# Kernel tuning notes

Measured on AMD Instinct MI355X. Metric: run time of the kernel, lower is better.

Reference implementation:

```python
import jax, jax.numpy as jnp
import numpy as np

HIDDEN = 128
EDGE_DIM = 32
N_NODES = 50000
N_EDGES = 800000


def setup_inputs() -> dict:
    key = jax.random.key(0)
    ks = jax.random.split(key, 8)
    node_features = jax.random.normal(ks[0], (N_NODES, HIDDEN), dtype=jnp.float32)
    edge_index = jax.random.randint(ks[1], (2, N_EDGES), 0, N_NODES, dtype=jnp.int64)
    edge_attr = jax.random.normal(ks[2], (N_EDGES, EDGE_DIM), dtype=jnp.float32)
    # parameters (Linear stored as [in, out] for x @ W + b)
    s_et = 1.0 / np.sqrt(EDGE_DIM)
    W_edge = jax.random.uniform(ks[3], (EDGE_DIM, HIDDEN), jnp.float32, -s_et, s_et)
    b_edge = jnp.zeros((HIDDEN,), jnp.float32)
    s1 = 1.0 / np.sqrt(3 * HIDDEN)
    W1 = jax.random.uniform(ks[4], (3 * HIDDEN, HIDDEN), jnp.float32, -s1, s1)
    b1 = jnp.zeros((HIDDEN,), jnp.float32)
    s2 = 1.0 / np.sqrt(HIDDEN)
    W2 = jax.random.uniform(ks[5], (HIDDEN, 1), jnp.float32, -s2, s2)
    b2 = jnp.zeros((1,), jnp.float32)
    return {
        "node_features": node_features,
        "edge_attr": edge_attr,
        "W_edge": W_edge, "b_edge": b_edge,
        "W1": W1, "b1": b1, "W2": W2, "b2": b2,
        "edge_index": edge_index,
    }


def reference(node_features, edge_attr, W_edge, b_edge, W1, b1, W2, b2, edge_index):
    row, col = edge_index[0], edge_index[1]
    src = node_features[row]                 # [E, H] gather
    dst = node_features[col]                 # [E, H] gather
    edge_feat = edge_attr @ W_edge + b_edge  # [E, H]
    combined = jnp.concatenate([src, edge_feat, dst], axis=-1)  # [E, 3H]
    h = jax.nn.relu(combined @ W1 + b1)      # [E, H]
    attn = jax.nn.sigmoid(h @ W2 + b2)       # [E, 1]
    return attn
```

## Files before the change

kernel.cpp:

```cpp
#include <hip/hip_runtime.h>
#include <hip/hip_bf16.h>

#define HIDDEN   128
#define EDGE_DIM 32
#define NNODE    50000
#define NEDGE    800000
#define KSTEPS   9
#define NFRAG    8
#define LDS_KS   8

typedef __attribute__((ext_vector_type(4))) float        f32x4;
typedef __attribute__((ext_vector_type(8))) short        bf16x8;
typedef __attribute__((ext_vector_type(4))) unsigned int u32x4;

#define BPACK_USHORTS  (KSTEPS * NFRAG * 64 * 8)
#define BIAS_OFF_BYTES (BPACK_USHORTS * 2)
#define FLAG_OFF_BYTES (BIAS_OFF_BYTES + 128 * 4)
#define DATA_OFF       74752

#define PP_OFF   DATA_OFF
#define QP_OFF   (PP_OFF + NNODE * HIDDEN * 2)
#define IDXN_OFF (QP_OFF + NNODE * HIDDEN * 2)
#define WS_NEW   (IDXN_OFF + 2 * NEDGE * 4)

#define NODE_OFF_BYTES DATA_OFF
#define IDX_OFF_BYTES  (NODE_OFF_BYTES + NNODE * HIDDEN * 2)
#define WS_R8          (IDX_OFF_BYTES + 2 * NEDGE * 4)

__device__ __forceinline__ unsigned short f2bf(float f) {
  unsigned u = __builtin_bit_cast(unsigned, f);
  u += 0x7FFFu + ((u >> 16) & 1u);
  return (unsigned short)(u >> 16);
}

__device__ __forceinline__ unsigned cvt_pk_bf16(float a, float b) {
  union { __hip_bfloat162 h; unsigned u; } cv;
  cv.h = __float22bfloat162_rn(make_float2(a, b));
  return cv.u;
}

__device__ __forceinline__ bf16x8 pack8(f32x4 lo, f32x4 hi) {
  u32x4 u;
  u[0] = cvt_pk_bf16(lo[0], lo[1]);
  u[1] = cvt_pk_bf16(lo[2], lo[3]);
  u[2] = cvt_pk_bf16(hi[0], hi[1]);
  u[3] = cvt_pk_bf16(hi[2], hi[3]);
  return __builtin_bit_cast(bf16x8, u);
}

__device__ __forceinline__ void gload_lds16(const void* g, void* l) {
  __builtin_amdgcn_global_load_lds(
      (const __attribute__((address_space(1))) unsigned int*)g,
      (__attribute__((address_space(3))) unsigned int*)l, 16, 0, 0);
}

#define MFMA(a, b, c) __builtin_amdgcn_mfma_f32_16x16x32_bf16((a), (b), (c), 0, 0, 0)

__global__ void setup_kernel(const float* __restrict__ W_edge,
                             const float* __restrict__ b_edge,
                             const float* __restrict__ W1,
                             const float* __restrict__ b1,
                             const void*  __restrict__ eidx,
                             unsigned short* __restrict__ Bpack,
                             float* __restrict__ bias_eff,
                             int*   __restrict__ flag64) {
  const int bid = blockIdx.x, tid = threadIdx.x;
  if (bid < 36) {
    const int pair  = bid * 2 + (tid >> 6);
    const int lane  = tid & 63;
    const int kstep = pair >> 3;
    const int f     = pair & 7;
    const int col   = f * 16 + (lane & 15);
    const int kbase = kstep * 32 + (lane >> 4) * 8;
    float vals[8];
#pragma unroll
    for (int j = 0; j < 8; ++j) {
      const int k = kbase + j;
      float val;
      if (k < 128) {
        val = W1[k * 128 + col];
      } else if (k < 256) {
        val = W1[(k + 128) * 128 + col];
      } else {
        const int kk = k - 256;
        float s = 0.f;
        for (int t = 0; t < 128; ++t)
          s = fmaf(W_edge[kk * 128 + t], W1[(128 + t) * 128 + col], s);
        val = s;
      }
      vals[j] = val;
    }
    u32x4 sv;
#pragma unroll
    for (int j = 0; j < 4; ++j)
      sv[j] = (unsigned)f2bf(vals[2 * j]) | ((unsigned)f2bf(vals[2 * j + 1]) << 16);
    *(u32x4*)(Bpack + ((kstep * NFRAG + f) * 64 + lane) * 8) = sv;
  } else {
    if (tid < 128) {
      float s = b1[tid];
      for (int t = 0; t < 128; ++t)
        s = fmaf(b_edge[t], W1[(128 + t) * 128 + tid], s);
      bias_eff[tid] = s;
    }
    if (tid == 0) {
      const unsigned* w = (const unsigned*)eidx;
      int all0 = 1;
      for (int i = 0; i < 64; ++i) all0 &= (w[2 * i + 1] == 0u) ? 1 : 0;
      *flag64 = all0;
    }
  }
}

__global__ __launch_bounds__(256) void cvt_nodes_kernel(const float* __restrict__ nodef,
                                                        unsigned short* __restrict__ nbf) {
  const int i = blockIdx.x * 256 + threadIdx.x;
  if (i >= NNODE * HIDDEN / 8) return;
  f32x4 lo = *(const f32x4*)(nodef + i * 8);
  f32x4 hi = *(const f32x4*)(nodef + i * 8 + 4);
  *(bf16x8*)(nbf + i * 8) = pack8(lo, hi);
}

__global__ __launch_bounds__(256) void cvt_idx_kernel(const void* __restrict__ eidx,
                                                      const int* __restrict__ flag64,
                                                      int* __restrict__ idx32) {
  const int i = blockIdx.x * 256 + threadIdx.x;
  if (i >= 2 * NEDGE) return;
  if (*flag64) idx32[i] = (int)((const long long*)eidx)[i];
  else         idx32[i] = ((const int*)eidx)[i];
}

__global__ __launch_bounds__(256, 3) void pq_kernel(
    const float* __restrict__ nodef,
    const unsigned short* __restrict__ Bpack,
    const float* __restrict__ bias_eff,
    unsigned* __restrict__ Pp,
    unsigned* __restrict__ Qp) {
  const int tid  = threadIdx.x;
  const int lane = tid & 63;
  const int wid  = tid >> 6;
  const int l15  = lane & 15;
  const int kg   = lane >> 4;
  const int nb   = blockIdx.x * 128 + wid * 32;

  const int n0 = min(nb + l15, NNODE - 1);
  const int n1 = min(nb + 16 + l15, NNODE - 1);
  bf16x8 a0[4], a1[4];
#pragma unroll
  for (int ks = 0; ks < 4; ++ks) {
    const float* p0 = nodef + (size_t)n0 * HIDDEN + ks * 32 + kg * 8;
    const float* p1 = nodef + (size_t)n1 * HIDDEN + ks * 32 + kg * 8;
    a0[ks] = pack8(*(const f32x4*)p0, *(const f32x4*)(p0 + 4));
    a1[ks] = pack8(*(const f32x4*)p1, *(const f32x4*)(p1 + 4));
  }

  float bv[NFRAG];
#pragma unroll
  for (int f = 0; f < NFRAG; ++f) bv[f] = bias_eff[f * 16 + l15];

  f32x4 acc[2][NFRAG];
#pragma unroll
  for (int m = 0; m < 2; ++m)
#pragma unroll
    for (int f = 0; f < NFRAG; ++f)
      acc[m][f] = (f32x4){bv[f], bv[f], bv[f], bv[f]};
#pragma unroll
  for (int ks = 0; ks < 4; ++ks)
#pragma unroll
    for (int f = 0; f < NFRAG; ++f) {
      bf16x8 bfr = *(const bf16x8*)(Bpack + ((ks * NFRAG + f) * 64 + lane) * 8);
      acc[0][f] = MFMA(a0[ks], bfr, acc[0][f]);
      acc[1][f] = MFMA(a1[ks], bfr, acc[1][f]);
    }
#pragma unroll
  for (int m = 0; m < 2; ++m)
#pragma unroll
    for (int r = 0; r < 4; ++r) {
      const int n = nb + m * 16 + kg * 4 + r;
      if (n < NNODE) {
        u32x4 sv;
#pragma unroll
        for (int k = 0; k < 4; ++k)
          sv[k] = cvt_pk_bf16(acc[m][2 * k][r], acc[m][2 * k + 1][r]);
        *(u32x4*)(Pp + (size_t)n * 64 + l15 * 4) = sv;
      }
    }

#pragma unroll
  for (int m = 0; m < 2; ++m)
#pragma unroll
    for (int f = 0; f < NFRAG; ++f)
      acc[m][f] = (f32x4){0.f, 0.f, 0.f, 0.f};
#pragma unroll
  for (int ks = 0; ks < 4; ++ks)
#pragma unroll
    for (int f = 0; f < NFRAG; ++f) {
      bf16x8 bfr = *(const bf16x8*)(Bpack + (((ks + 4) * NFRAG + f) * 64 + lane) * 8);
      acc[0][f] = MFMA(a0[ks], bfr, acc[0][f]);
      acc[1][f] = MFMA(a1[ks], bfr, acc[1][f]);
    }
#pragma unroll
  for (int m = 0; m < 2; ++m)
#pragma unroll
    for (int r = 0; r < 4; ++r) {
      const int n = nb + m * 16 + kg * 4 + r;
      if (n < NNODE) {
        u32x4 sv;
#pragma unroll
        for (int k = 0; k < 4; ++k)
          sv[k] = cvt_pk_bf16(acc[m][2 * k][r], acc[m][2 * k + 1][r]);
        *(u32x4*)(Qp + (size_t)n * 64 + l15 * 4) = sv;
      }
    }
}

__global__ __launch_bounds__(256, 3) void edge_attn_pq(
    const float* __restrict__ eattr,
    const int*   __restrict__ idx32,
    const unsigned* __restrict__ Pp,
    const unsigned* __restrict__ Qp,
    const unsigned short* __restrict__ Bpack,
    const float* __restrict__ W2,
    const float* __restrict__ b2,
    float* __restrict__ out) {
  const int tid   = threadIdx.x;
  const int lane  = tid & 63;
  const int wid   = tid >> 6;
  const int l15   = lane & 15;
  const int kg    = lane >> 4;
  const int ebase = blockIdx.x * 128 + wid * 32;

  const f32x4 zero4 = {0.f, 0.f, 0.f, 0.f};

  int rn[2][4], cn[2][4];
#pragma unroll
  for (int m = 0; m < 2; ++m)
#pragma unroll
    for (int r = 0; r < 4; ++r) {
      rn[m][r] = idx32[ebase + m * 16 + kg * 4 + r];
      cn[m][r] = idx32[NEDGE + ebase + m * 16 + kg * 4 + r];
    }

  u32x4 pu[2][4], qu[2][4];
#pragma unroll
  for (int m = 0; m < 2; ++m)
#pragma unroll
    for (int r = 0; r < 4; ++r)
      pu[m][r] = *(const u32x4*)(Pp + (size_t)rn[m][r] * 64 + l15 * 4);
#pragma unroll
  for (int m = 0; m < 2; ++m)
#pragma unroll
    for (int r = 0; r < 4; ++r)
      qu[m][r] = *(const u32x4*)(Qp + (size_t)cn[m][r] * 64 + l15 * 4);

  bf16x8 ae0, ae1;
  {
    const float* pe = eattr + (size_t)(ebase + l15) * EDGE_DIM + kg * 8;
    ae0 = pack8(*(const f32x4*)pe, *(const f32x4*)(pe + 4));
  }
  {
    const float* pe = eattr + (size_t)(ebase + 16 + l15) * EDGE_DIM + kg * 8;
    ae1 = pack8(*(const f32x4*)pe, *(const f32x4*)(pe + 4));
  }

  float w2v[NFRAG];
#pragma unroll
  for (int f = 0; f < NFRAG; ++f) w2v[f] = W2[f * 16 + l15];
  const float bias2 = b2[0];

  f32x4 acc[2][NFRAG];
#pragma unroll
  for (int f = 0; f < NFRAG; ++f) {
    bf16x8 bfr = *(const bf16x8*)(Bpack + ((8 * NFRAG + f) * 64 + lane) * 8);
    acc[0][f] = MFMA(ae0, bfr, zero4);
    acc[1][f] = MFMA(ae1, bfr, zero4);
  }

#pragma unroll
  for (int m = 0; m < 2; ++m)
#pragma unroll
    for (int r = 0; r < 4; ++r)
#pragma unroll
      for (int k = 0; k < 4; ++k) {
        const unsigned up = pu[m][r][k];
        acc[m][2 * k][r]     += __builtin_bit_cast(float, up << 16);
        acc[m][2 * k + 1][r] += __builtin_bit_cast(float, up & 0xffff0000u);
      }
#pragma unroll
  for (int m = 0; m < 2; ++m)
#pragma unroll
    for (int r = 0; r < 4; ++r)
#pragma unroll
      for (int k = 0; k < 4; ++k) {
        const unsigned uq = qu[m][r][k];
        acc[m][2 * k][r]     += __builtin_bit_cast(float, uq << 16);
        acc[m][2 * k + 1][r] += __builtin_bit_cast(float, uq & 0xffff0000u);
      }

  float part[2][4];
#pragma unroll
  for (int m = 0; m < 2; ++m)
#pragma unroll
    for (int rr = 0; rr < 4; ++rr) {
      float s = 0.f;
#pragma unroll
      for (int f = 0; f < NFRAG; ++f) {
        float h = fmaxf(acc[m][f][rr], 0.f);
        s = fmaf(h, w2v[f], s);
      }
      part[m][rr] = s;
    }

#pragma unroll
  for (int mask = 1; mask < 16; mask <<= 1)
#pragma unroll
    for (int m = 0; m < 2; ++m)
#pragma unroll
      for (int rr = 0; rr < 4; ++rr)
        part[m][rr] += __shfl_xor(part[m][rr], mask, 64);

  if (l15 == 0) {
#pragma unroll
    for (int m = 0; m < 2; ++m)
#pragma unroll
      for (int rr = 0; rr < 4; ++rr) {
        float x = part[m][rr] + bias2;
        out[ebase + m * 16 + kg * 4 + rr] = 1.f / (1.f + __expf(-x));
      }
  }
}

__global__ __launch_bounds__(512, 4) void edge_attn_kernel(
    const unsigned short* __restrict__ nbf,
    const float* __restrict__ eattr,
    const int*   __restrict__ idx32,
    const unsigned short* __restrict__ Bpack,
    const float* __restrict__ bias_eff,
    const float* __restrict__ W2,
    const float* __restrict__ b2,
    float* __restrict__ out) {
  __shared__ unsigned short lds_b[LDS_KS * NFRAG * 64 * 8];

  const int tid   = threadIdx.x;
  const int lane  = tid & 63;
  const int wid   = tid >> 6;
  const int l15   = lane & 15;
  const int kg    = lane >> 4;
  const int ebase = blockIdx.x * 256 + wid * 32;

#pragma unroll
  for (int i = 0; i < 8; ++i) {
    const char* g = (const char*)Bpack + (size_t)(i * 512 + tid) * 16;
    char*       l = (char*)lds_b + (size_t)(i * 512 + wid * 64) * 16;
    gload_lds16(g, l);
  }

  const int r0 = idx32[ebase + l15];
  const int r1 = idx32[ebase + 16 + l15];
  const int c0 = idx32[NEDGE + ebase + l15];
  const int c1 = idx32[NEDGE + ebase + 16 + l15];

  bf16x8 a0[4], a1[4];
#pragma unroll
  for (int ks = 0; ks < 4; ++ks) {
    a0[ks] = *(const bf16x8*)(nbf + (size_t)r0 * HIDDEN + kg * 8 + ks * 32);
    a1[ks] = *(const bf16x8*)(nbf + (size_t)r1 * HIDDEN + kg * 8 + ks * 32);
  }

  __syncthreads();

  f32x4 acc[2][NFRAG];
#pragma unroll
  for (int m = 0; m < 2; ++m)
#pragma unroll
    for (int f = 0; f < NFRAG; ++f)
      acc[m][f] = (f32x4){0.f, 0.f, 0.f, 0.f};

#pragma unroll
  for (int ks = 0; ks < 4; ++ks)
#pragma unroll
    for (int f = 0; f < NFRAG; ++f) {
      bf16x8 bfr = *(const bf16x8*)(lds_b + ((ks * NFRAG + f) * 64 + lane) * 8);
      acc[0][f] = MFMA(a0[ks], bfr, acc[0][f]);
      acc[1][f] = MFMA(a1[ks], bfr, acc[1][f]);
    }

  __builtin_amdgcn_sched_barrier(0);

#pragma unroll
  for (int ks = 0; ks < 4; ++ks) {
    a0[ks] = *(const bf16x8*)(nbf + (size_t)c0 * HIDDEN + kg * 8 + ks * 32);
    a1[ks] = *(const bf16x8*)(nbf + (size_t)c1 * HIDDEN + kg * 8 + ks * 32);
  }

#pragma unroll
  for (int ks = 0; ks < 4; ++ks)
#pragma unroll
    for (int f = 0; f < NFRAG; ++f) {
      bf16x8 bfr = *(const bf16x8*)(lds_b + (((ks + 4) * NFRAG + f) * 64 + lane) * 8);
      acc[0][f] = MFMA(a0[ks], bfr, acc[0][f]);
      acc[1][f] = MFMA(a1[ks], bfr, acc[1][f]);
    }

  __builtin_amdgcn_sched_barrier(0);

  bf16x8 ae0, ae1;
  {
    const float* pe = eattr + (size_t)(ebase + l15) * EDGE_DIM + kg * 8;
    ae0 = pack8(*(const f32x4*)pe, *(const f32x4*)(pe + 4));
  }
  {
    const float* pe = eattr + (size_t)(ebase + 16 + l15) * EDGE_DIM + kg * 8;
    ae1 = pack8(*(const f32x4*)pe, *(const f32x4*)(pe + 4));
  }
#pragma unroll
  for (int f = 0; f < NFRAG; ++f) {
    bf16x8 bfr = *(const bf16x8*)(Bpack + ((8 * NFRAG + f) * 64 + lane) * 8);
    acc[0][f] = MFMA(ae0, bfr, acc[0][f]);
    acc[1][f] = MFMA(ae1, bfr, acc[1][f]);
  }

  float w2v[NFRAG], bv[NFRAG];
#pragma unroll
  for (int f = 0; f < NFRAG; ++f) {
    w2v[f] = W2[f * 16 + l15];
    bv[f]  = bias_eff[f * 16 + l15];
  }
  const float bias2 = b2[0];

  float part[2][4];
#pragma unroll
  for (int m = 0; m < 2; ++m)
#pragma unroll
    for (int rr = 0; rr < 4; ++rr) {
      float s = 0.f;
#pragma unroll
      for (int f = 0; f < NFRAG; ++f) {
        float h = fmaxf(acc[m][f][rr] + bv[f], 0.f);
        s = fmaf(h, w2v[f], s);
      }
      part[m][rr] = s;
    }

#pragma unroll
  for (int mask = 1; mask < 16; mask <<= 1)
#pragma unroll
    for (int m = 0; m < 2; ++m)
#pragma unroll
      for (int rr = 0; rr < 4; ++rr)
        part[m][rr] += __shfl_xor(part[m][rr], mask, 64);

  if (l15 == 0) {
#pragma unroll
    for (int m = 0; m < 2; ++m)
#pragma unroll
      for (int rr = 0; rr < 4; ++rr) {
        float x = part[m][rr] + bias2;
        out[ebase + m * 16 + kg * 4 + rr] = 1.f / (1.f + __expf(-x));
      }
  }
}

__global__ __launch_bounds__(256) void edge_attn_kernel_fp32(
    const float* __restrict__ nodef,
    const float* __restrict__ eattr,
    const void*  __restrict__ eidx,
    const unsigned short* __restrict__ Bpack,
    const float* __restrict__ bias_eff,
    const float* __restrict__ W2,
    const float* __restrict__ b2,
    const int*   __restrict__ flag64,
    float* __restrict__ out) {
  const int lane  = threadIdx.x & 63;
  const int wid   = threadIdx.x >> 6;
  const int ebase = blockIdx.x * 128 + wid * 32;
  const int l15   = lane & 15;
  const int kg    = lane >> 4;
  const int koff  = kg * 8;
  const int e0 = ebase + l15;
  const int e1 = e0 + 16;

  long r0, c0, r1, c1;
  if (*flag64) {
    const long long* p = (const long long*)eidx;
    r0 = (long)p[e0];          r1 = (long)p[e1];
    c0 = (long)p[NEDGE + e0];  c1 = (long)p[NEDGE + e1];
  } else {
    const int* p = (const int*)eidx;
    r0 = p[e0];          r1 = p[e1];
    c0 = p[NEDGE + e0];  c1 = p[NEDGE + e1];
  }

  f32x4 acc[2][NFRAG];
#pragma unroll
  for (int m = 0; m < 2; ++m)
#pragma unroll
    for (int f = 0; f < NFRAG; ++f)
      acc[m][f] = (f32x4){0.f, 0.f, 0.f, 0.f};

#pragma unroll 1
  for (int ks = 0; ks < KSTEPS; ++ks) {
    const float *p0, *p1;
    if (ks < 4)      { p0 = nodef + r0 * HIDDEN + ks * 32;       p1 = nodef + r1 * HIDDEN + ks * 32; }
    else if (ks < 8) { p0 = nodef + c0 * HIDDEN + (ks - 4) * 32; p1 = nodef + c1 * HIDDEN + (ks - 4) * 32; }
    else             { p0 = eattr + (long)e0 * EDGE_DIM;         p1 = eattr + (long)e1 * EDGE_DIM; }

    f32x4 lo0 = *(const f32x4*)(p0 + koff);
    f32x4 hi0 = *(const f32x4*)(p0 + koff + 4);
    f32x4 lo1 = *(const f32x4*)(p1 + koff);
    f32x4 hi1 = *(const f32x4*)(p1 + koff + 4);
    bf16x8 a0 = pack8(lo0, hi0);
    bf16x8 a1 = pack8(lo1, hi1);

#pragma unroll
    for (int f = 0; f < NFRAG; ++f) {
      bf16x8 bfr = *(const bf16x8*)(Bpack + ((ks * NFRAG + f) * 64 + lane) * 8);
      acc[0][f] = MFMA(a0, bfr, acc[0][f]);
      acc[1][f] = MFMA(a1, bfr, acc[1][f]);
    }
  }

  float w2v[NFRAG], bv[NFRAG];
#pragma unroll
  for (int f = 0; f < NFRAG; ++f) {
    w2v[f] = W2[f * 16 + l15];
    bv[f]  = bias_eff[f * 16 + l15];
  }
  const float bias2 = b2[0];

  float part[2][4];
#pragma unroll
  for (int m = 0; m < 2; ++m)
#pragma unroll
    for (int r = 0; r < 4; ++r) {
      float s = 0.f;
#pragma unroll
      for (int f = 0; f < NFRAG; ++f) {
        float h = acc[m][f][r] + bv[f];
        h = fmaxf(h, 0.f);
        s = fmaf(h, w2v[f], s);
      }
      part[m][r] = s;
    }

#pragma unroll
  for (int mask = 1; mask < 16; mask <<= 1)
#pragma unroll
    for (int m = 0; m < 2; ++m)
#pragma unroll
      for (int r = 0; r < 4; ++r)
        part[m][r] += __shfl_xor(part[m][r], mask, 64);

  if (l15 == 0) {
#pragma unroll
    for (int m = 0; m < 2; ++m)
#pragma unroll
      for (int r = 0; r < 4; ++r) {
        float x = part[m][r] + bias2;
        out[ebase + m * 16 + kg * 4 + r] = 1.f / (1.f + __expf(-x));
      }
  }
}

extern "C" void kernel_launch(void* const* d_in, const int* in_sizes, int n_in,
                              void* d_out, int out_size, void* d_ws, size_t ws_size,
                              hipStream_t stream) {
  const float* nodef  = (const float*)d_in[0];
  const float* eattr  = (const float*)d_in[1];
  const float* W_edge = (const float*)d_in[2];
  const float* b_edge = (const float*)d_in[3];
  const float* W1     = (const float*)d_in[4];
  const float* b1     = (const float*)d_in[5];
  const float* W2     = (const float*)d_in[6];
  const float* b2     = (const float*)d_in[7];
  const void*  eidx   = d_in[8];

  unsigned short* Bpack    = (unsigned short*)d_ws;
  float*          bias_eff = (float*)((char*)d_ws + BIAS_OFF_BYTES);
  int*            flag64   = (int*)((char*)d_ws + FLAG_OFF_BYTES);

  setup_kernel<<<dim3(37), dim3(128), 0, stream>>>(W_edge, b_edge, W1, b1, eidx,
                                                   Bpack, bias_eff, flag64);

  if (ws_size >= (size_t)WS_NEW) {
    unsigned* Pp    = (unsigned*)((char*)d_ws + PP_OFF);
    unsigned* Qp    = (unsigned*)((char*)d_ws + QP_OFF);
    int*      idx32 = (int*)((char*)d_ws + IDXN_OFF);
    cvt_idx_kernel<<<dim3((2 * NEDGE + 255) / 256), dim3(256), 0, stream>>>(eidx, flag64, idx32);
    pq_kernel<<<dim3((NNODE + 127) / 128), dim3(256), 0, stream>>>(nodef, Bpack, bias_eff, Pp, Qp);
    edge_attn_pq<<<dim3(NEDGE / 128), dim3(256), 0, stream>>>(
        eattr, idx32, Pp, Qp, Bpack, W2, b2, (float*)d_out);
  } else if (ws_size >= (size_t)WS_R8) {
    unsigned short* nbf   = (unsigned short*)((char*)d_ws + NODE_OFF_BYTES);
    int*            idx32 = (int*)((char*)d_ws + IDX_OFF_BYTES);
    cvt_idx_kernel<<<dim3((2 * NEDGE + 255) / 256), dim3(256), 0, stream>>>(eidx, flag64, idx32);
    cvt_nodes_kernel<<<dim3((NNODE * HIDDEN / 8 + 255) / 256), dim3(256), 0, stream>>>(nodef, nbf);
    edge_attn_kernel<<<dim3(NEDGE / 256), dim3(512), 0, stream>>>(
        nbf, eattr, idx32, Bpack, bias_eff, W2, b2, (float*)d_out);
  } else {
    edge_attn_kernel_fp32<<<dim3(NEDGE / 128), dim3(256), 0, stream>>>(
        nodef, eattr, eidx, Bpack, bias_eff, W2, b2, flag64, (float*)d_out);
  }
}
```

Baseline: 117.5 us.

## Fuse index conversion into edge kernel and stage PQ weights in LDS

The edge kernel now reads the int64/int32 edge indices directly, with the width chosen by a flag, and the separate index-conversion kernel launch and its intermediate buffer are removed. pq_kernel now uses 512-thread blocks that load the 64 KB packed weight matrix into LDS through direct global-to-LDS loads, so MFMA operands come from shared memory rather than global memory. The edge kernel raises its occupancy hint and moves the P/Q gathers after the edge-attr loads. The cost is 8-byte index reads inside the edge kernel, a 64 KB LDS footprint per pq block, and more register pressure from the higher occupancy target.

```diff
diff --git a/kernel.cpp b/kernel.cpp
--- a/kernel.cpp
+++ b/kernel.cpp
@@ -20,8 +20,7 @@
 
 #define PP_OFF   DATA_OFF
 #define QP_OFF   (PP_OFF + NNODE * HIDDEN * 2)
-#define IDXN_OFF (QP_OFF + NNODE * HIDDEN * 2)
-#define WS_NEW   (IDXN_OFF + 2 * NEDGE * 4)
+#define WS_NEW   (QP_OFF + NNODE * HIDDEN * 2)
 
 #define NODE_OFF_BYTES DATA_OFF
 #define IDX_OFF_BYTES  (NODE_OFF_BYTES + NNODE * HIDDEN * 2)
@@ -129,18 +128,27 @@
   else         idx32[i] = ((const int*)eidx)[i];
 }
 
-__global__ __launch_bounds__(256, 3) void pq_kernel(
+__global__ __launch_bounds__(512, 2) void pq_kernel(
     const float* __restrict__ nodef,
     const unsigned short* __restrict__ Bpack,
     const float* __restrict__ bias_eff,
     unsigned* __restrict__ Pp,
     unsigned* __restrict__ Qp) {
+  __shared__ unsigned short lds_b[LDS_KS * NFRAG * 64 * 8];
+
   const int tid  = threadIdx.x;
   const int lane = tid & 63;
   const int wid  = tid >> 6;
   const int l15  = lane & 15;
   const int kg   = lane >> 4;
-  const int nb   = blockIdx.x * 128 + wid * 32;
+  const int nb   = blockIdx.x * 256 + wid * 32;
+
+#pragma unroll
+  for (int i = 0; i < 8; ++i) {
+    const char* g = (const char*)Bpack + (size_t)(i * 512 + tid) * 16;
+    char*       l = (char*)lds_b + (size_t)(i * 512 + wid * 64) * 16;
+    gload_lds16(g, l);
+  }
 
   const int n0 = min(nb + l15, NNODE - 1);
   const int n1 = min(nb + 16 + l15, NNODE - 1);
@@ -157,6 +165,8 @@
 #pragma unroll
   for (int f = 0; f < NFRAG; ++f) bv[f] = bias_eff[f * 16 + l15];
 
+  __syncthreads();
+
   f32x4 acc[2][NFRAG];
 #pragma unroll
   for (int m = 0; m < 2; ++m)
@@ -167,7 +177,7 @@
   for (int ks = 0; ks < 4; ++ks)
 #pragma unroll
     for (int f = 0; f < NFRAG; ++f) {
-      bf16x8 bfr = *(const bf16x8*)(Bpack + ((ks * NFRAG + f) * 64 + lane) * 8);
+      bf16x8 bfr = *(const bf16x8*)(lds_b + ((ks * NFRAG + f) * 64 + lane) * 8);
       acc[0][f] = MFMA(a0[ks], bfr, acc[0][f]);
       acc[1][f] = MFMA(a1[ks], bfr, acc[1][f]);
     }
@@ -194,7 +204,7 @@
   for (int ks = 0; ks < 4; ++ks)
 #pragma unroll
     for (int f = 0; f < NFRAG; ++f) {
-      bf16x8 bfr = *(const bf16x8*)(Bpack + (((ks + 4) * NFRAG + f) * 64 + lane) * 8);
+      bf16x8 bfr = *(const bf16x8*)(lds_b + (((ks + 4) * NFRAG + f) * 64 + lane) * 8);
       acc[0][f] = MFMA(a0[ks], bfr, acc[0][f]);
       acc[1][f] = MFMA(a1[ks], bfr, acc[1][f]);
     }
@@ -213,9 +223,10 @@
     }
 }
 
-__global__ __launch_bounds__(256, 3) void edge_attn_pq(
+__global__ __launch_bounds__(256, 6) void edge_attn_pq(
     const float* __restrict__ eattr,
-    const int*   __restrict__ idx32,
+    const void*  __restrict__ eidx,
+    const int*   __restrict__ flag64,
     const unsigned* __restrict__ Pp,
     const unsigned* __restrict__ Qp,
     const unsigned short* __restrict__ Bpack,
@@ -232,25 +243,27 @@
   const f32x4 zero4 = {0.f, 0.f, 0.f, 0.f};
 
   int rn[2][4], cn[2][4];
-#pragma unroll
-  for (int m = 0; m < 2; ++m)
-#pragma unroll
-    for (int r = 0; r < 4; ++r) {
-      rn[m][r] = idx32[ebase + m * 16 + kg * 4 + r];
-      cn[m][r] = idx32[NEDGE + ebase + m * 16 + kg * 4 + r];
-    }
-
-  u32x4 pu[2][4], qu[2][4];
-#pragma unroll
-  for (int m = 0; m < 2; ++m)
-#pragma unroll
-    for (int r = 0; r < 4; ++r)
-      pu[m][r] = *(const u32x4*)(Pp + (size_t)rn[m][r] * 64 + l15 * 4);
-#pragma unroll
-  for (int m = 0; m < 2; ++m)
-#pragma unroll
-    for (int r = 0; r < 4; ++r)
-      qu[m][r] = *(const u32x4*)(Qp + (size_t)cn[m][r] * 64 + l15 * 4);
+  if (*flag64) {
+    const long long* p = (const long long*)eidx;
+#pragma unroll
+    for (int m = 0; m < 2; ++m)
+#pragma unroll
+      for (int r = 0; r < 4; ++r) {
+        const int e = ebase + m * 16 + kg * 4 + r;
+        rn[m][r] = (int)p[e];
+        cn[m][r] = (int)p[NEDGE + e];
+      }
+  } else {
+    const int* p = (const int*)eidx;
+#pragma unroll
+    for (int m = 0; m < 2; ++m)
+#pragma unroll
+      for (int r = 0; r < 4; ++r) {
+        const int e = ebase + m * 16 + kg * 4 + r;
+        rn[m][r] = p[e];
+        cn[m][r] = p[NEDGE + e];
+      }
+  }
 
   bf16x8 ae0, ae1;
   {
@@ -261,11 +274,22 @@
     const float* pe = eattr + (size_t)(ebase + 16 + l15) * EDGE_DIM + kg * 8;
     ae1 = pack8(*(const f32x4*)pe, *(const f32x4*)(pe + 4));
   }
-
   float w2v[NFRAG];
 #pragma unroll
   for (int f = 0; f < NFRAG; ++f) w2v[f] = W2[f * 16 + l15];
   const float bias2 = b2[0];
+
+  u32x4 pu[2][4], qu[2][4];
+#pragma unroll
+  for (int m = 0; m < 2; ++m)
+#pragma unroll
+    for (int r = 0; r < 4; ++r)
+      pu[m][r] = *(const u32x4*)(Pp + (size_t)rn[m][r] * 64 + l15 * 4);
+#pragma unroll
+  for (int m = 0; m < 2; ++m)
+#pragma unroll
+    for (int r = 0; r < 4; ++r)
+      qu[m][r] = *(const u32x4*)(Qp + (size_t)cn[m][r] * 64 + l15 * 4);
 
   f32x4 acc[2][NFRAG];
 #pragma unroll
@@ -582,13 +606,11 @@
                                                    Bpack, bias_eff, flag64);
 
   if (ws_size >= (size_t)WS_NEW) {
-    unsigned* Pp    = (unsigned*)((char*)d_ws + PP_OFF);
-    unsigned* Qp    = (unsigned*)((char*)d_ws + QP_OFF);
-    int*      idx32 = (int*)((char*)d_ws + IDXN_OFF);
-    cvt_idx_kernel<<<dim3((2 * NEDGE + 255) / 256), dim3(256), 0, stream>>>(eidx, flag64, idx32);
-    pq_kernel<<<dim3((NNODE + 127) / 128), dim3(256), 0, stream>>>(nodef, Bpack, bias_eff, Pp, Qp);
+    unsigned* Pp = (unsigned*)((char*)d_ws + PP_OFF);
+    unsigned* Qp = (unsigned*)((char*)d_ws + QP_OFF);
+    pq_kernel<<<dim3((NNODE + 255) / 256), dim3(512), 0, stream>>>(nodef, Bpack, bias_eff, Pp, Qp);
     edge_attn_pq<<<dim3(NEDGE / 128), dim3(256), 0, stream>>>(
-        eattr, idx32, Pp, Qp, Bpack, W2, b2, (float*)d_out);
+        eattr, eidx, flag64, Pp, Qp, Bpack, W2, b2, (float*)d_out);
   } else if (ws_size >= (size_t)WS_R8) {
     unsigned short* nbf   = (unsigned short*)((char*)d_ws + NODE_OFF_BYTES);
     int*            idx32 = (int*)((char*)d_ws + IDX_OFF_BYTES);
```

Result: slower. 335.5 us (+185.6%).
